# Performance work log

Hardware: AMD Instinct MI355X
Metric: run time of the kernel (lower is better)

Reference implementation:

```python
import jax, jax.numpy as jnp
import numpy as np

N_NODES = 30000
N_EDGES = 480000
IN_SIZE = 256
EDGE_FEAT = 32
N_TOWERS = 4
DELTA = 2.5


def setup_inputs():
    key = jax.random.key(0)
    ks = jax.random.split(key, 8)
    T, d = N_TOWERS, IN_SIZE // N_TOWERS
    m_in = 2 * d + EDGE_FEAT                 # M: Linear(2*tower_in+edge_feat -> tower_in)
    u_in = (4 * 3 + 1) * d                   # U: Linear((n_agg*n_scaler+1)*tower_in -> tower_out)
    return {
        "n_feat": jax.random.normal(ks[0], (N_NODES, IN_SIZE), jnp.float32),
        "e_feat": jax.random.normal(ks[1], (N_EDGES, EDGE_FEAT), jnp.float32),
        "src": jax.random.randint(ks[2], (N_EDGES,), 0, N_NODES),
        "dst": jax.random.randint(ks[3], (N_EDGES,), 0, N_NODES),
        "M_w": jax.random.normal(ks[4], (T, d, m_in), jnp.float32) * (1.0 / np.sqrt(m_in)),
        "M_b": jnp.zeros((T, d), jnp.float32),
        "U_w": jax.random.normal(ks[5], (T, d, u_in), jnp.float32) * (1.0 / np.sqrt(u_in)),
        "U_b": jnp.zeros((T, d), jnp.float32),
        "bn_gamma": jnp.ones((T, d), jnp.float32),
        "bn_beta": jnp.zeros((T, d), jnp.float32),
        "mix_w": jax.random.normal(ks[6], (IN_SIZE, IN_SIZE), jnp.float32) * (1.0 / np.sqrt(IN_SIZE)),
        "mix_b": jnp.zeros((IN_SIZE,), jnp.float32),
    }


def reference(n_feat, e_feat, src, dst, M_w, M_b, U_w, U_b, bn_gamma, bn_beta, mix_w, mix_b):
    N, F = n_feat.shape
    T, d, _ = M_w.shape
    E = src.shape[0]
    h = n_feat.reshape(N, T, d)                                   # towers split the feature dim
    ef = jnp.broadcast_to(e_feat[:, None, :], (E, T, e_feat.shape[1]))
    f = jnp.concatenate([h[src], h[dst], ef], axis=-1)            # [E,T,2d+ef]
    msg = jnp.einsum('eti,toi->eto', f, M_w) + M_b                # per-edge message, [E,T,d]

    deg = jax.ops.segment_sum(jnp.ones((E,), msg.dtype), dst, num_segments=N)  # in-degree
    degc = jnp.maximum(deg, 1.0)[:, None, None]
    s = jax.ops.segment_sum(msg, dst, num_segments=N)
    ssq = jax.ops.segment_sum(msg * msg, dst, num_segments=N)
    mean = s / degc
    var = jax.nn.relu(ssq / degc - mean * mean)                   # DGL aggregate_var
    std = jnp.sqrt(var + 1e-30)                                   # DGL aggregate_std
    has = (deg > 0.0)[:, None, None]
    mx = jnp.where(has, jax.ops.segment_max(msg, dst, num_segments=N), 0.0)
    mn = jnp.where(has, jax.ops.segment_min(msg, dst, num_segments=N), 0.0)
    agg = jnp.concatenate([mean, mx, mn, std], axis=-1)           # [N,T,4d]

    logd = jnp.log(deg + 1.0)
    amp = (logd / DELTA)[:, None, None]                            # amplification scaler
    att = jnp.where(deg > 0.0, DELTA / jnp.maximum(logd, 1e-12), 0.0)[:, None, None]  # attenuation
    hsc = jnp.concatenate([agg, agg * amp, agg * att], axis=-1)   # [N,T,12d]

    u_in = jnp.concatenate([h, hsc], axis=-1)                     # [N,T,13d]
    u = jnp.einsum('nti,toi->nto', u_in, U_w) + U_b               # [N,T,d]
    mu = jnp.mean(u, axis=0)
    v = jnp.mean((u - mu) ** 2, axis=0)
    u = (u - mu) / jnp.sqrt(v + 1e-5) * bn_gamma + bn_beta        # BatchNorm1d (training mode)

    h_cat = u.reshape(N, F)
    mixed = h_cat @ mix_w.T + mix_b
    mixed = jnp.where(mixed > 0, mixed, 0.01 * mixed)             # LeakyReLU mixing layer
    out = mixed + n_feat                                          # residual (in_size==out_size)
    return jax.nn.relu(out)                                       # last == 0 -> ReLU
```

## Files before the change

### kernel.cpp

```cpp
#include <hip/hip_runtime.h>
#include <math.h>

constexpr float DELTA_ = 2.5f;
#define BN_BLOCKS 512

typedef __attribute__((ext_vector_type(8))) short bf16x8;
typedef __attribute__((ext_vector_type(4))) float f32x4;
typedef __attribute__((ext_vector_type(2))) _Float16 half2_t;

#if defined(__has_builtin)
#if __has_builtin(__builtin_amdgcn_fdot2)
#define DOT2(a,b,c) __builtin_amdgcn_fdot2((a),(b),(c),false)
#endif
#endif
#ifndef DOT2
#define DOT2(a,b,c) fmaf((float)(a).x,(float)(b).x, fmaf((float)(a).y,(float)(b).y,(c)))
#endif

__device__ inline ushort bf16h(float x){
  union { float f; unsigned u; } v; v.f = x;
  unsigned r = v.u + 0x7fffu + ((v.u >> 16) & 1u);
  return (ushort)(r >> 16);
}
__device__ inline float bf16f(ushort h){
  union { unsigned u; float f; } v; v.u = ((unsigned)h) << 16;
  return v.f;
}

__global__ __launch_bounds__(256) void k_tU(const float* __restrict__ Uw, ushort* __restrict__ Wpk2){
  int i = blockIdx.x*256 + threadIdx.x;
  if (i >= 4*192*320) return;
  int k   = i % 320;
  int col = (i/320) % 192;
  int t   = i/(320*192);
  int path = col >> 6, o = col & 63;
  float v = 0.f;
  int src = -1;
  if (k < 64){ if (path == 0) src = k; }
  else        src = k + path*256;
  if (src >= 0) v = Uw[((size_t)(t*64 + o))*832 + src];
  Wpk2[i] = bf16h(v);
}

__global__ __launch_bounds__(256) void k_tMm(const float* __restrict__ mixw, ushort* __restrict__ Wm2){
  int i = blockIdx.x*256 + threadIdx.x;
  if (i >= 256*256) return;
  Wm2[i] = bf16h(mixw[i]);
}

__global__ __launch_bounds__(256) void k_tE(const float* __restrict__ Mw, _Float16* __restrict__ Mwefh){
  int i = blockIdx.x*256 + threadIdx.x;
  if (i >= 256*32) return;
  int k = i & 31, c = i >> 5;
  Mwefh[i] = (_Float16)Mw[(size_t)c*160 + 128 + k];
}

__global__ __launch_bounds__(256) void k_xh(const float* __restrict__ nf, ushort* __restrict__ X2, int N){
  for (long i = blockIdx.x*256 + threadIdx.x; i < (long)N*256; i += (long)gridDim.x*256){
    int n = (int)(i >> 8), c = (int)(i & 255);
    int t = c >> 6, d = c & 63;
    int j = d >> 3, pos = d & 7;
    float v = nf[i];
    ushort hi = bf16h(v);
    size_t base = (((size_t)n*4 + t)*40 + j)*16;
    X2[base + pos]     = hi;
    X2[base + 8 + pos] = bf16h(v - bf16f(hi));
  }
}

__global__ __launch_bounds__(256) void k_hist(const int* __restrict__ dstv, int* __restrict__ cnt, int E){
  int e = blockIdx.x*256 + threadIdx.x;
  if (e < E) atomicAdd(&cnt[dstv[e]], 1);
}

__global__ __launch_bounds__(256) void k_scan1(const int* __restrict__ cnt, int* __restrict__ offs,
                                               int* __restrict__ bsum, int N){
  __shared__ int lds[256];
  int i = threadIdx.x;
  int g = blockIdx.x*256 + i;
  int v = (g < N) ? cnt[g] : 0;
  int acc = v;
  lds[i] = acc; __syncthreads();
  for (int s = 1; s < 256; s <<= 1){
    int t = (i >= s) ? lds[i - s] : 0;
    __syncthreads();
    acc += t; lds[i] = acc;
    __syncthreads();
  }
  if (g < N) offs[g] = acc - v;
  if (i == 255) bsum[blockIdx.x] = acc;
}

__global__ __launch_bounds__(256) void k_scan2(int* __restrict__ bsum, int NB){
  __shared__ int lds[256];
  int i = threadIdx.x;
  int v = (i < NB) ? bsum[i] : 0;
  int acc = v;
  lds[i] = acc; __syncthreads();
  for (int s = 1; s < 256; s <<= 1){
    int t = (i >= s) ? lds[i - s] : 0;
    __syncthreads();
    acc += t; lds[i] = acc;
    __syncthreads();
  }
  if (i < NB) bsum[i] = acc - v;
}

__global__ __launch_bounds__(256) void k_scan3(int* __restrict__ offs, const int* __restrict__ bsum, int N, int E){
  int g = blockIdx.x*256 + threadIdx.x;
  if (g < N) offs[g] += bsum[blockIdx.x];
  if (g == 0) offs[N] = E;
}

__global__ __launch_bounds__(256) void k_fill(const int* __restrict__ dstv, const int* __restrict__ offs,
                                              int* __restrict__ cur, int* __restrict__ elist, int E){
  int e = blockIdx.x*256 + threadIdx.x;
  if (e < E){
    int d = dstv[e];
    elist[offs[d] + atomicAdd(&cur[d], 1)] = e;
  }
}

__global__ __launch_bounds__(256) void k_perm(const int* __restrict__ elist, const int* __restrict__ srcv,
                                              const float* __restrict__ efeat,
                                              int* __restrict__ esrc, _Float16* __restrict__ efh, int E){
  int g = blockIdx.x*256 + threadIdx.x;
  int pos = g >> 3;
  int q   = g & 7;
  if (pos >= E) return;
  int e = elist[pos];
  if (q == 0) esrc[pos] = srcv[e];
  float4 v = *(const float4*)(efeat + (size_t)e*32 + q*4);
  union { ushort4 u; _Float16 h[4]; } cv;
  cv.h[0] = (_Float16)v.x; cv.h[1] = (_Float16)v.y;
  cv.h[2] = (_Float16)v.z; cv.h[3] = (_Float16)v.w;
  *(ushort4*)(efh + (size_t)pos*32 + q*4) = cv.u;
}

__global__ __launch_bounds__(256) void k_ab(const float* __restrict__ nf, const float* __restrict__ Mw,
                                            const float* __restrict__ Mb,
                                            _Float16* __restrict__ A_h, float* __restrict__ B, int N){
  int c = threadIdx.x;
  int t = __builtin_amdgcn_readfirstlane(threadIdx.x >> 6);
  float ws[64], wd[64];
  const float* row = Mw + (size_t)c*160;
#pragma unroll
  for (int k = 0; k < 64; k += 4){
    float4 a = *(const float4*)(row + k);
    float4 b = *(const float4*)(row + 64 + k);
    ws[k]=a.x; ws[k+1]=a.y; ws[k+2]=a.z; ws[k+3]=a.w;
    wd[k]=b.x; wd[k+1]=b.y; wd[k+2]=b.z; wd[k+3]=b.w;
  }
  float bias = Mb[c];
  for (int n = blockIdx.x; n < N; n += gridDim.x){
    const float* h = nf + (size_t)n*256 + t*64;
    float sa = 0.f, sb = 0.f;
#pragma unroll
    for (int k = 0; k < 64; k += 4){
      float4 h4 = *(const float4*)(h + k);
      sa = fmaf(ws[k], h4.x, sa);  sb = fmaf(wd[k], h4.x, sb);
      sa = fmaf(ws[k+1], h4.y, sa); sb = fmaf(wd[k+1], h4.y, sb);
      sa = fmaf(ws[k+2], h4.z, sa); sb = fmaf(wd[k+2], h4.z, sb);
      sa = fmaf(ws[k+3], h4.w, sa); sb = fmaf(wd[k+3], h4.w, sb);
    }
    A_h[(size_t)n*256 + c] = (_Float16)sa;
    B[(size_t)n*256 + c] = sb + bias;
  }
}

__global__ __launch_bounds__(256) void k_agg(const int* __restrict__ offs, const int* __restrict__ esrc,
                                             const _Float16* __restrict__ efh,
                                             const _Float16* __restrict__ A_h, const float* __restrict__ B,
                                             const _Float16* __restrict__ Mwefh,
                                             ushort* __restrict__ X2, float* __restrict__ sc, int N){
  int c = threadIdx.x;
  union Wu { int4 i[4]; half2_t h[16]; } wr;
  {
    const int4* wp = (const int4*)(Mwefh + (size_t)c*32);
    wr.i[0] = wp[0]; wr.i[1] = wp[1]; wr.i[2] = wp[2]; wr.i[3] = wp[3];
  }

  int n = blockIdx.x;
  if (n >= N) return;
  int o0 = __builtin_amdgcn_readfirstlane(offs[n]);
  int o1 = __builtin_amdgcn_readfirstlane(offs[n+1]);
  int cnt = o1 - o0;
  float b0 = B[(size_t)n*256 + c];
  float s = 0.f, ss = 0.f, mx = -__builtin_huge_valf(), mn = __builtin_huge_valf();

  union Eu { int4 i[4]; half2_t h[16]; };

  int i = 0;
  for (; i + 4 <= cnt; i += 4){
    int p = o0 + i;
    int s0 = __builtin_amdgcn_readfirstlane(esrc[p+0]);
    int s1 = __builtin_amdgcn_readfirstlane(esrc[p+1]);
    int s2 = __builtin_amdgcn_readfirstlane(esrc[p+2]);
    int s3 = __builtin_amdgcn_readfirstlane(esrc[p+3]);
    Eu e0, e1, e2, e3;
    {
      const int4* p0 = (const int4*)(efh + (size_t)(p+0)*32);
      const int4* p1 = (const int4*)(efh + (size_t)(p+1)*32);
      const int4* p2 = (const int4*)(efh + (size_t)(p+2)*32);
      const int4* p3 = (const int4*)(efh + (size_t)(p+3)*32);
#pragma unroll
      for (int q = 0; q < 4; ++q){ e0.i[q]=p0[q]; e1.i[q]=p1[q]; e2.i[q]=p2[q]; e3.i[q]=p3[q]; }
    }
    float a0 = (float)A_h[(size_t)s0*256 + c];
    float a1 = (float)A_h[(size_t)s1*256 + c];
    float a2 = (float)A_h[(size_t)s2*256 + c];
    float a3 = (float)A_h[(size_t)s3*256 + c];
    float m0 = b0 + a0;
    float m1 = b0 + a1;
    float m2 = b0 + a2;
    float m3 = b0 + a3;
#pragma unroll
    for (int q = 0; q < 16; ++q){
      m0 = DOT2(e0.h[q], wr.h[q], m0);
      m1 = DOT2(e1.h[q], wr.h[q], m1);
      m2 = DOT2(e2.h[q], wr.h[q], m2);
      m3 = DOT2(e3.h[q], wr.h[q], m3);
    }
    s += m0; s += m1; s += m2; s += m3;
    ss = fmaf(m0, m0, ss); ss = fmaf(m1, m1, ss);
    ss = fmaf(m2, m2, ss); ss = fmaf(m3, m3, ss);
    mx = fmaxf(mx, fmaxf(fmaxf(m0, m1), fmaxf(m2, m3)));
    mn = fminf(mn, fminf(fminf(m0, m1), fminf(m2, m3)));
  }
  for (; i < cnt; ++i){
    int p = o0 + i;
    int sidx = __builtin_amdgcn_readfirstlane(esrc[p]);
    Eu e0;
    {
      const int4* p0 = (const int4*)(efh + (size_t)p*32);
#pragma unroll
      for (int q = 0; q < 4; ++q) e0.i[q] = p0[q];
    }
    float m = b0 + (float)A_h[(size_t)sidx*256 + c];
#pragma unroll
    for (int q = 0; q < 16; ++q) m = DOT2(e0.h[q], wr.h[q], m);
    s += m;
    ss = fmaf(m, m, ss);
    mx = fmaxf(mx, m);
    mn = fminf(mn, m);
  }

  float deg  = (float)cnt;
  float degc = fmaxf(deg, 1.f);
  float inv  = 1.f / degc;
  float mean = s * inv;
  float var  = fmaxf(ss * inv - mean*mean, 0.f);
  float sd   = sqrtf(var + 1e-30f);
  if (cnt == 0){ mx = 0.f; mn = 0.f; }

  int t = c >> 6, d = c & 63;
#define PUTX(SLOT, VAL) { int kk = 64 + (SLOT)*64 + d; int jj = kk >> 3, pp = kk & 7;      \
    size_t base = (((size_t)n*4 + t)*40 + jj)*16;                                          \
    ushort hi = bf16h(VAL);                                                                \
    X2[base + pp] = hi; X2[base + 8 + pp] = bf16h((VAL) - bf16f(hi)); }
  PUTX(0, mean) PUTX(1, mx) PUTX(2, mn) PUTX(3, sd)
#undef PUTX
  if (c == 0){
    float logd = logf(deg + 1.f);
    sc[(size_t)n*2]     = logd * (1.f / DELTA_);
    sc[(size_t)n*2 + 1] = (cnt > 0) ? (DELTA_ / fmaxf(logd, 1e-12f)) : 0.f;
  }
}

__global__ __launch_bounds__(256) void k_u(const ushort* __restrict__ X2, const ushort* __restrict__ Wpk2,
                                           const float* __restrict__ sc, const float* __restrict__ Ub,
                                           float* __restrict__ uout, int Nn){
  __shared__ float su[64][68];
  int tid = threadIdx.x;
  int t   = blockIdx.y;
  int nbase = blockIdx.x*64;
  int lane = tid & 63, wv = tid >> 6;
  int li = lane & 15, kc = lane >> 4;
  int cbase = wv*48;

  f32x4 acc[4][3];
#pragma unroll
  for (int ri = 0; ri < 4; ++ri)
#pragma unroll
    for (int ci = 0; ci < 3; ++ci) acc[ri][ci] = (f32x4)0.f;

  const ushort* wb = Wpk2 + (size_t)t*192*320;

#pragma unroll 2
  for (int kt = 0; kt < 10; ++kt){
    bf16x8 ah[4], al[4], bh[3];
#pragma unroll
    for (int ri = 0; ri < 4; ++ri){
      int row = nbase + ri*16 + li;
      if (row >= Nn) row = Nn - 1;
      const ushort* ap = X2 + (((size_t)row*4 + t)*40 + kt*4 + kc)*16;
      ah[ri] = *(const bf16x8*)(ap);
      al[ri] = *(const bf16x8*)(ap + 8);
    }
#pragma unroll
    for (int ci = 0; ci < 3; ++ci){
      int col = cbase + ci*16 + li;
      bh[ci] = *(const bf16x8*)(wb + (size_t)col*320 + kt*32 + kc*8);
    }
#pragma unroll
    for (int ci = 0; ci < 3; ++ci)
#pragma unroll
      for (int ri = 0; ri < 4; ++ri){
        acc[ri][ci] = __builtin_amdgcn_mfma_f32_16x16x32_bf16(ah[ri], bh[ci], acc[ri][ci], 0, 0, 0);
        acc[ri][ci] = __builtin_amdgcn_mfma_f32_16x16x32_bf16(al[ri], bh[ci], acc[ri][ci], 0, 0, 0);
      }
  }

#define Y1_STORE(CI, OB) { _Pragma("unroll") for (int ri = 0; ri < 4; ++ri)               \
    { _Pragma("unroll") for (int r = 0; r < 4; ++r)                                        \
      su[ri*16 + kc*4 + r][(OB) + li] = acc[ri][CI][r]; } }
#define Y_ADD(CI, OB, SCOFF) { _Pragma("unroll") for (int ri = 0; ri < 4; ++ri)           \
    { _Pragma("unroll") for (int r = 0; r < 4; ++r){                                       \
      int node = ri*16 + kc*4 + r;                                                        \
      int gn = nbase + node; int gnc = (gn < Nn) ? gn : (Nn - 1);                          \
      float scl = sc[(size_t)gnc*2 + (SCOFF)];                                            \
      su[node][(OB) + li] += scl * acc[ri][CI][r]; } } }

  if (wv == 0){ Y1_STORE(0, 0)  Y1_STORE(1, 16) Y1_STORE(2, 32) }
  else if (wv == 1){ Y1_STORE(0, 48) }
  __syncthreads();
  if (wv == 1){ Y_ADD(1, 0, 0)  Y_ADD(2, 16, 0) }
  else if (wv == 2){ Y_ADD(0, 32, 0) Y_ADD(1, 48, 0) }
  __syncthreads();
  if (wv == 2){ Y_ADD(2, 0, 1) }
  else if (wv == 3){ Y_ADD(0, 16, 1) Y_ADD(1, 32, 1) Y_ADD(2, 48, 1) }
  __syncthreads();
#undef Y1_STORE
#undef Y_ADD

  for (int idx = tid; idx < 64*16; idx += 256){
    int n = idx >> 4, o4 = (idx & 15)*4;
    int gn = nbase + n;
    if (gn < Nn){
      float4 v = *(float4*)(&su[n][o4]);
      const float* ubp = Ub + t*64 + o4;
      v.x += ubp[0]; v.y += ubp[1]; v.z += ubp[2]; v.w += ubp[3];
      *(float4*)(&uout[(size_t)gn*256 + t*64 + o4]) = v;
    }
  }
}

__global__ __launch_bounds__(256) void k_bnstat(const float* __restrict__ u, float* __restrict__ part, int N){
  int c = threadIdx.x;
  int b = blockIdx.x;
  float s = 0.f, ss = 0.f;
  for (int n = b; n < N; n += gridDim.x){
    float v = u[(size_t)n*256 + c];
    s += v;
    ss = fmaf(v, v, ss);
  }
  part[(size_t)b*512 + c]       = s;
  part[(size_t)b*512 + 256 + c] = ss;
}

__global__ __launch_bounds__(256) void k_bnfin(const float* __restrict__ part, const float* __restrict__ gam,
                                               const float* __restrict__ bet, float* __restrict__ bnsc, int N){
  int c = threadIdx.x;
  float s = 0.f, ss = 0.f;
  for (int b = 0; b < BN_BLOCKS; ++b){
    s  += part[(size_t)b*512 + c];
    ss += part[(size_t)b*512 + 256 + c];
  }
  float invN = 1.f / (float)N;
  float mu  = s * invN;
  float ex2 = ss * invN;
  float var = fmaxf(ex2 - mu*mu, 0.f);
  float inv = 1.f / sqrtf(var + 1e-5f);
  float scale = gam[c] * inv;
  bnsc[c]       = scale;
  bnsc[256 + c] = bet[c] - mu*scale;
}

__global__ __launch_bounds__(256) void k_xm(const float* __restrict__ u, const float* __restrict__ bnsc,
                                            ushort* __restrict__ X2m, int N){
  for (long i = blockIdx.x*256 + threadIdx.x; i < (long)N*256; i += (long)gridDim.x*256){
    int n = (int)(i >> 8), c = (int)(i & 255);
    float v = fmaf(u[i], bnsc[c], bnsc[256 + c]);
    int j = c >> 3, pos = c & 7;
    size_t base = ((size_t)n*32 + j)*16;
    ushort hi = bf16h(v);
    X2m[base + pos]     = hi;
    X2m[base + 8 + pos] = bf16h(v - bf16f(hi));
  }
}

__global__ __launch_bounds__(256) void k_mix(const ushort* __restrict__ X2m, const ushort* __restrict__ Wm2,
                                             const float* __restrict__ mixb, const float* __restrict__ nf,
                                             float* __restrict__ outp, int Nn){
  int tid = threadIdx.x;
  int nbase = blockIdx.x*64;
  int lane = tid & 63, wv = tid >> 6;
  int li = lane & 15, kc = lane >> 4;

  f32x4 acc[4][4];
#pragma unroll
  for (int ri = 0; ri < 4; ++ri)
#pragma unroll
    for (int ci = 0; ci < 4; ++ci) acc[ri][ci] = (f32x4)0.f;

#pragma unroll 2
  for (int kt = 0; kt < 8; ++kt){
    bf16x8 ah[4], al[4], bh[4];
#pragma unroll
    for (int ri = 0; ri < 4; ++ri){
      int row = nbase + ri*16 + li;
      if (row >= Nn) row = Nn - 1;
      const ushort* ap = X2m + (((size_t)row*32 + kt*4 + kc))*16;
      ah[ri] = *(const bf16x8*)(ap);
      al[ri] = *(const bf16x8*)(ap + 8);
    }
#pragma unroll
    for (int ci = 0; ci < 4; ++ci){
      int col = wv*64 + ci*16 + li;
      bh[ci] = *(const bf16x8*)(Wm2 + (size_t)col*256 + kt*32 + kc*8);
    }
#pragma unroll
    for (int ci = 0; ci < 4; ++ci)
#pragma unroll
      for (int ri = 0; ri < 4; ++ri){
        acc[ri][ci] = __builtin_amdgcn_mfma_f32_16x16x32_bf16(ah[ri], bh[ci], acc[ri][ci], 0, 0, 0);
        acc[ri][ci] = __builtin_amdgcn_mfma_f32_16x16x32_bf16(al[ri], bh[ci], acc[ri][ci], 0, 0, 0);
      }
  }

#pragma unroll
  for (int ri = 0; ri < 4; ++ri){
#pragma unroll
    for (int r = 0; r < 4; ++r){
      int node = ri*16 + kc*4 + r;
      int gn = nbase + node;
      if (gn < Nn){
#pragma unroll
        for (int ci = 0; ci < 4; ++ci){
          int col = wv*64 + ci*16 + li;
          float m = acc[ri][ci][r] + mixb[col];
          m = (m > 0.f) ? m : 0.01f*m;
          float o = m + nf[(size_t)gn*256 + col];
          outp[(size_t)gn*256 + col] = fmaxf(o, 0.f);
        }
      }
    }
  }
}

extern "C" void kernel_launch(void* const* d_in, const int* in_sizes, int n_in,
                              void* d_out, int out_size, void* d_ws, size_t ws_size,
                              hipStream_t stream){
  const float* nf   = (const float*)d_in[0];
  const float* ef   = (const float*)d_in[1];
  const int*   srcv = (const int*)  d_in[2];
  const int*   dstv = (const int*)  d_in[3];
  const float* Mw   = (const float*)d_in[4];
  const float* Mb   = (const float*)d_in[5];
  const float* Uw   = (const float*)d_in[6];
  const float* Ub   = (const float*)d_in[7];
  const float* gam  = (const float*)d_in[8];
  const float* bet  = (const float*)d_in[9];
  const float* mixw = (const float*)d_in[10];
  const float* mixb = (const float*)d_in[11];
  int N = in_sizes[0] / 256;
  int E = in_sizes[2];
  float* out = (float*)d_out;

  char* wp = (char*)d_ws;
  auto alloc = [&](size_t bytes){
    char* p = wp;
    wp += (bytes + 1023) & ~(size_t)1023;
    return (void*)p;
  };
  int*      cnt   = (int*)     alloc((size_t)N*4);
  int*      offs  = (int*)     alloc((size_t)(N+1)*4);
  int*      cur   = (int*)     alloc((size_t)N*4);
  int*      bsum  = (int*)     alloc(256*4);
  int*      elist = (int*)     alloc((size_t)E*4);
  int*      esrc  = (int*)     alloc((size_t)E*4);
  size_t ealias   = (size_t)E*32*2;
  size_t malias   = (size_t)N*512*2;
  char*     shbuf = (char*)    alloc(ealias > malias ? ealias : malias);
  _Float16* efh   = (_Float16*)shbuf;
  ushort*   X2m   = (ushort*)  shbuf;
  _Float16* A_h   = (_Float16*)alloc((size_t)N*256*2);
  float*    B     = (float*)   alloc((size_t)N*256*4);
  float*    sc    = (float*)   alloc((size_t)N*2*4);
  float*    part  = (float*)   alloc((size_t)BN_BLOCKS*512*4);
  float*    bnsc  = (float*)   alloc(512*4);
  ushort*   X2    = (ushort*)  alloc((size_t)N*4*40*16*2);
  ushort*   Wpk2  = (ushort*)  alloc((size_t)4*192*320*2);
  ushort*   Wm2   = (ushort*)  alloc((size_t)256*256*2);
  _Float16* Mwefh = (_Float16*)alloc((size_t)256*32*2);

  hipMemsetAsync(cnt,  0, (size_t)N*4,  stream);
  hipMemsetAsync(cur,  0, (size_t)N*4,  stream);

  k_tU  <<<(4*192*320 + 255)/256, 256, 0, stream>>>(Uw, Wpk2);
  k_tMm <<<(256*256 + 255)/256, 256, 0, stream>>>(mixw, Wm2);
  k_tE  <<<(256*32 + 255)/256, 256, 0, stream>>>(Mw, Mwefh);
  k_hist<<<(E + 255)/256, 256, 0, stream>>>(dstv, cnt, E);
  k_ab  <<<2048, 256, 0, stream>>>(nf, Mw, Mb, A_h, B, N);
  k_xh  <<<2048, 256, 0, stream>>>(nf, X2, N);

  int NB = (N + 255)/256;
  k_scan1<<<NB, 256, 0, stream>>>(cnt, offs, bsum, N);
  k_scan2<<<1, 256, 0, stream>>>(bsum, NB);
  k_scan3<<<NB, 256, 0, stream>>>(offs, bsum, N, E);
  k_fill <<<(E + 255)/256, 256, 0, stream>>>(dstv, offs, cur, elist, E);
  k_perm <<<(E*8 + 255)/256, 256, 0, stream>>>(elist, srcv, ef, esrc, efh, E);

  k_agg<<<N, 256, 0, stream>>>(offs, esrc, efh, A_h, B, Mwefh, X2, sc, N);

  dim3 ugrid((N + 63)/64, 4);
  k_u<<<ugrid, 256, 0, stream>>>(X2, Wpk2, sc, Ub, out, N);

  k_bnstat<<<BN_BLOCKS, 256, 0, stream>>>(out, part, N);
  k_bnfin <<<1, 256, 0, stream>>>(part, gam, bet, bnsc, N);
  k_xm   <<<2048, 256, 0, stream>>>(out, bnsc, X2m, N);
  k_mix  <<<(N + 63)/64, 256, 0, stream>>>(X2m, Wm2, mixb, nf, out, N);
}
```

Before: 493.8 us.

## Use MFMA for edge-feature messages, fold split into k_ab, fuse BN stats into k_u

```diff
diff --git a/kernel.cpp b/kernel.cpp
--- a/kernel.cpp
+++ b/kernel.cpp
@@ -2,20 +2,10 @@
 #include <math.h>
 
 constexpr float DELTA_ = 2.5f;
-#define BN_BLOCKS 512
 
 typedef __attribute__((ext_vector_type(8))) short bf16x8;
+typedef __attribute__((ext_vector_type(8))) _Float16 f16x8;
 typedef __attribute__((ext_vector_type(4))) float f32x4;
-typedef __attribute__((ext_vector_type(2))) _Float16 half2_t;
-
-#if defined(__has_builtin)
-#if __has_builtin(__builtin_amdgcn_fdot2)
-#define DOT2(a,b,c) __builtin_amdgcn_fdot2((a),(b),(c),false)
-#endif
-#endif
-#ifndef DOT2
-#define DOT2(a,b,c) fmaf((float)(a).x,(float)(b).x, fmaf((float)(a).y,(float)(b).y,(c)))
-#endif
 
 __device__ inline ushort bf16h(float x){
   union { float f; unsigned u; } v; v.f = x;
@@ -48,24 +38,15 @@
   Wm2[i] = bf16h(mixw[i]);
 }
 
-__global__ __launch_bounds__(256) void k_tE(const float* __restrict__ Mw, _Float16* __restrict__ Mwefh){
+__global__ __launch_bounds__(256) void k_tE2(const float* __restrict__ Mw, _Float16* __restrict__ Wefp){
   int i = blockIdx.x*256 + threadIdx.x;
-  if (i >= 256*32) return;
-  int k = i & 31, c = i >> 5;
-  Mwefh[i] = (_Float16)Mw[(size_t)c*160 + 128 + k];
-}
-
-__global__ __launch_bounds__(256) void k_xh(const float* __restrict__ nf, ushort* __restrict__ X2, int N){
-  for (long i = blockIdx.x*256 + threadIdx.x; i < (long)N*256; i += (long)gridDim.x*256){
-    int n = (int)(i >> 8), c = (int)(i & 255);
-    int t = c >> 6, d = c & 63;
-    int j = d >> 3, pos = d & 7;
-    float v = nf[i];
-    ushort hi = bf16h(v);
-    size_t base = (((size_t)n*4 + t)*40 + j)*16;
-    X2[base + pos]     = hi;
-    X2[base + 8 + pos] = bf16h(v - bf16f(hi));
-  }
+  if (i >= 16*64*8) return;
+  int j    = i & 7;
+  int lane = (i >> 3) & 63;
+  int cb   = i >> 9;
+  int ch = cb*16 + (lane & 15);
+  int k  = ((lane >> 4) & 3)*8 + j;
+  Wefp[i] = (_Float16)Mw[(size_t)ch*160 + 128 + k];
 }
 
 __global__ __launch_bounds__(256) void k_hist(const int* __restrict__ dstv, int* __restrict__ cnt, int E){
@@ -139,7 +120,8 @@
 
 __global__ __launch_bounds__(256) void k_ab(const float* __restrict__ nf, const float* __restrict__ Mw,
                                             const float* __restrict__ Mb,
-                                            _Float16* __restrict__ A_h, float* __restrict__ B, int N){
+                                            _Float16* __restrict__ A_h, float* __restrict__ B,
+                                            ushort* __restrict__ X2, int N){
   int c = threadIdx.x;
   int t = __builtin_amdgcn_readfirstlane(threadIdx.x >> 6);
   float ws[64], wd[64];
@@ -165,102 +147,112 @@
     }
     A_h[(size_t)n*256 + c] = (_Float16)sa;
     B[(size_t)n*256 + c] = sb + bias;
+    float v = nf[(size_t)n*256 + c];
+    ushort hi = bf16h(v);
+    int d = c & 63, j = d >> 3, pp = d & 7;
+    size_t base = (((size_t)n*4 + t)*40 + j)*16;
+    X2[base + pp]     = hi;
+    X2[base + 8 + pp] = bf16h(v - bf16f(hi));
   }
 }
 
 __global__ __launch_bounds__(256) void k_agg(const int* __restrict__ offs, const int* __restrict__ esrc,
                                              const _Float16* __restrict__ efh,
                                              const _Float16* __restrict__ A_h, const float* __restrict__ B,
-                                             const _Float16* __restrict__ Mwefh,
-                                             ushort* __restrict__ X2, float* __restrict__ sc, int N){
-  int c = threadIdx.x;
-  union Wu { int4 i[4]; half2_t h[16]; } wr;
-  {
-    const int4* wp = (const int4*)(Mwefh + (size_t)c*32);
-    wr.i[0] = wp[0]; wr.i[1] = wp[1]; wr.i[2] = wp[2]; wr.i[3] = wp[3];
-  }
-
+                                             const _Float16* __restrict__ Wefp,
+                                             ushort* __restrict__ X2, float* __restrict__ sc, int N, int E){
   int n = blockIdx.x;
   if (n >= N) return;
-  int o0 = __builtin_amdgcn_readfirstlane(offs[n]);
-  int o1 = __builtin_amdgcn_readfirstlane(offs[n+1]);
+  int tid = threadIdx.x;
+  int lane = tid & 63, wv = tid >> 6;
+  int li = lane & 15, kq = lane >> 4;
+
+  int o0 = offs[n], o1 = offs[n+1];
   int cnt = o1 - o0;
-  float b0 = B[(size_t)n*256 + c];
-  float s = 0.f, ss = 0.f, mx = -__builtin_huge_valf(), mn = __builtin_huge_valf();
-
-  union Eu { int4 i[4]; half2_t h[16]; };
-
-  int i = 0;
-  for (; i + 4 <= cnt; i += 4){
-    int p = o0 + i;
-    int s0 = __builtin_amdgcn_readfirstlane(esrc[p+0]);
-    int s1 = __builtin_amdgcn_readfirstlane(esrc[p+1]);
-    int s2 = __builtin_amdgcn_readfirstlane(esrc[p+2]);
-    int s3 = __builtin_amdgcn_readfirstlane(esrc[p+3]);
-    Eu e0, e1, e2, e3;
-    {
-      const int4* p0 = (const int4*)(efh + (size_t)(p+0)*32);
-      const int4* p1 = (const int4*)(efh + (size_t)(p+1)*32);
-      const int4* p2 = (const int4*)(efh + (size_t)(p+2)*32);
-      const int4* p3 = (const int4*)(efh + (size_t)(p+3)*32);
-#pragma unroll
-      for (int q = 0; q < 4; ++q){ e0.i[q]=p0[q]; e1.i[q]=p1[q]; e2.i[q]=p2[q]; e3.i[q]=p3[q]; }
-    }
-    float a0 = (float)A_h[(size_t)s0*256 + c];
-    float a1 = (float)A_h[(size_t)s1*256 + c];
-    float a2 = (float)A_h[(size_t)s2*256 + c];
-    float a3 = (float)A_h[(size_t)s3*256 + c];
-    float m0 = b0 + a0;
-    float m1 = b0 + a1;
-    float m2 = b0 + a2;
-    float m3 = b0 + a3;
-#pragma unroll
-    for (int q = 0; q < 16; ++q){
-      m0 = DOT2(e0.h[q], wr.h[q], m0);
-      m1 = DOT2(e1.h[q], wr.h[q], m1);
-      m2 = DOT2(e2.h[q], wr.h[q], m2);
-      m3 = DOT2(e3.h[q], wr.h[q], m3);
-    }
-    s += m0; s += m1; s += m2; s += m3;
-    ss = fmaf(m0, m0, ss); ss = fmaf(m1, m1, ss);
-    ss = fmaf(m2, m2, ss); ss = fmaf(m3, m3, ss);
-    mx = fmaxf(mx, fmaxf(fmaxf(m0, m1), fmaxf(m2, m3)));
-    mn = fminf(mn, fminf(fminf(m0, m1), fminf(m2, m3)));
-  }
-  for (; i < cnt; ++i){
-    int p = o0 + i;
-    int sidx = __builtin_amdgcn_readfirstlane(esrc[p]);
-    Eu e0;
-    {
-      const int4* p0 = (const int4*)(efh + (size_t)p*32);
-#pragma unroll
-      for (int q = 0; q < 4; ++q) e0.i[q] = p0[q];
-    }
-    float m = b0 + (float)A_h[(size_t)sidx*256 + c];
-#pragma unroll
-    for (int q = 0; q < 16; ++q) m = DOT2(e0.h[q], wr.h[q], m);
-    s += m;
-    ss = fmaf(m, m, ss);
-    mx = fmaxf(mx, m);
-    mn = fminf(mn, m);
-  }
-
-  float deg  = (float)cnt;
-  float degc = fmaxf(deg, 1.f);
-  float inv  = 1.f / degc;
-  float mean = s * inv;
-  float var  = fmaxf(ss * inv - mean*mean, 0.f);
-  float sd   = sqrtf(var + 1e-30f);
-  if (cnt == 0){ mx = 0.f; mn = 0.f; }
-
-  int t = c >> 6, d = c & 63;
-#define PUTX(SLOT, VAL) { int kk = 64 + (SLOT)*64 + d; int jj = kk >> 3, pp = kk & 7;      \
-    size_t base = (((size_t)n*4 + t)*40 + jj)*16;                                          \
-    ushort hi = bf16h(VAL);                                                                \
-    X2[base + pp] = hi; X2[base + 8 + pp] = bf16h((VAL) - bf16f(hi)); }
-  PUTX(0, mean) PUTX(1, mx) PUTX(2, mn) PUTX(3, sd)
+
+  f16x8 bf[4];
+#pragma unroll
+  for (int cbl = 0; cbl < 4; ++cbl)
+    bf[cbl] = *(const f16x8*)(Wefp + ((size_t)(wv*4 + cbl)*64 + lane)*8);
+
+  float b0[4];
+#pragma unroll
+  for (int cbl = 0; cbl < 4; ++cbl)
+    b0[cbl] = B[(size_t)n*256 + wv*64 + cbl*16 + li];
+
+  float s[4]  = {0.f,0.f,0.f,0.f};
+  float ss[4] = {0.f,0.f,0.f,0.f};
+  float mx[4], mn[4];
+#pragma unroll
+  for (int cbl = 0; cbl < 4; ++cbl){
+    mx[cbl] = -__builtin_huge_valf();
+    mn[cbl] =  __builtin_huge_valf();
+  }
+
+  for (int p = o0; p < o1; p += 16){
+    int posa = p + li; if (posa > E - 1) posa = E - 1;
+    f16x8 af = *(const f16x8*)(efh + (size_t)posa*32 + kq*8);
+    f32x4 ep0 = __builtin_amdgcn_mfma_f32_16x16x32_f16(af, bf[0], (f32x4)0.f, 0, 0, 0);
+    f32x4 ep1 = __builtin_amdgcn_mfma_f32_16x16x32_f16(af, bf[1], (f32x4)0.f, 0, 0, 0);
+    f32x4 ep2 = __builtin_amdgcn_mfma_f32_16x16x32_f16(af, bf[2], (f32x4)0.f, 0, 0, 0);
+    f32x4 ep3 = __builtin_amdgcn_mfma_f32_16x16x32_f16(af, bf[3], (f32x4)0.f, 0, 0, 0);
+#pragma unroll
+    for (int r = 0; r < 4; ++r){
+      int pr = p + kq*4 + r;
+      if (pr < o1){
+        int srcn = esrc[pr];
+        const _Float16* ap = A_h + (size_t)srcn*256 + wv*64 + li;
+        float a0 = (float)ap[0];
+        float a1 = (float)ap[16];
+        float a2 = (float)ap[32];
+        float a3 = (float)ap[48];
+        float m0 = ep0[r] + a0;
+        float m1 = ep1[r] + a1;
+        float m2 = ep2[r] + a2;
+        float m3 = ep3[r] + a3;
+        s[0] += m0; ss[0] = fmaf(m0, m0, ss[0]); mx[0] = fmaxf(mx[0], m0); mn[0] = fminf(mn[0], m0);
+        s[1] += m1; ss[1] = fmaf(m1, m1, ss[1]); mx[1] = fmaxf(mx[1], m1); mn[1] = fminf(mn[1], m1);
+        s[2] += m2; ss[2] = fmaf(m2, m2, ss[2]); mx[2] = fmaxf(mx[2], m2); mn[2] = fminf(mn[2], m2);
+        s[3] += m3; ss[3] = fmaf(m3, m3, ss[3]); mx[3] = fmaxf(mx[3], m3); mn[3] = fminf(mn[3], m3);
+      }
+    }
+  }
+
+#pragma unroll
+  for (int cbl = 0; cbl < 4; ++cbl){
+    s[cbl]  += __shfl_xor(s[cbl], 16);  s[cbl]  += __shfl_xor(s[cbl], 32);
+    ss[cbl] += __shfl_xor(ss[cbl], 16); ss[cbl] += __shfl_xor(ss[cbl], 32);
+    mx[cbl] = fmaxf(mx[cbl], __shfl_xor(mx[cbl], 16));
+    mx[cbl] = fmaxf(mx[cbl], __shfl_xor(mx[cbl], 32));
+    mn[cbl] = fminf(mn[cbl], __shfl_xor(mn[cbl], 16));
+    mn[cbl] = fminf(mn[cbl], __shfl_xor(mn[cbl], 32));
+  }
+
+  if (lane < 16){
+    float deg  = (float)cnt;
+    float degc = fmaxf(deg, 1.f);
+    float inv  = 1.f / degc;
+#pragma unroll
+    for (int cbl = 0; cbl < 4; ++cbl){
+      float b = b0[cbl];
+      float S  = fmaf(deg, b, s[cbl]);
+      float SS = fmaf(deg, b*b, fmaf(2.f*b, s[cbl], ss[cbl]));
+      float mean = S * inv;
+      float var  = fmaxf(SS * inv - mean*mean, 0.f);
+      float sd   = sqrtf(var + 1e-30f);
+      float MX = (cnt > 0) ? (b + mx[cbl]) : 0.f;
+      float MN = (cnt > 0) ? (b + mn[cbl]) : 0.f;
+      int d = cbl*16 + li;
+#define PUTX(SLOT, VAL) { int kk = 64 + (SLOT)*64 + d; int jj = kk >> 3, pp = kk & 7;     \
+      size_t base = (((size_t)n*4 + wv)*40 + jj)*16;                                       \
+      ushort hi2 = bf16h(VAL);                                                             \
+      X2[base + pp] = hi2; X2[base + 8 + pp] = bf16h((VAL) - bf16f(hi2)); }
+      PUTX(0, mean) PUTX(1, MX) PUTX(2, MN) PUTX(3, sd)
 #undef PUTX
-  if (c == 0){
+    }
+  }
+  if (tid == 0){
+    float deg = (float)cnt;
     float logd = logf(deg + 1.f);
     sc[(size_t)n*2]     = logd * (1.f / DELTA_);
     sc[(size_t)n*2 + 1] = (cnt > 0) ? (DELTA_ / fmaxf(logd, 1e-12f)) : 0.f;
@@ -269,8 +261,10 @@
 
 __global__ __launch_bounds__(256) void k_u(const ushort* __restrict__ X2, const ushort* __restrict__ Wpk2,
                                            const float* __restrict__ sc, const float* __restrict__ Ub,
-                                           float* __restrict__ uout, int Nn){
+                                           float* __restrict__ uout, float* __restrict__ part,
+                                           int Nn, int NBLK){
   __shared__ float su[64][68];
+  __shared__ float pbn[2][4][64];
   int tid = threadIdx.x;
   int t   = blockIdx.y;
   int nbase = blockIdx.x*64;
@@ -343,28 +337,41 @@
       *(float4*)(&uout[(size_t)gn*256 + t*64 + o4]) = v;
     }
   }
-}
-
-__global__ __launch_bounds__(256) void k_bnstat(const float* __restrict__ u, float* __restrict__ part, int N){
+
+  {
+    int cl = tid & 63, grp = tid >> 6;
+    float ubv = Ub[t*64 + cl];
+    float ps = 0.f, pss = 0.f;
+#pragma unroll
+    for (int q = 0; q < 16; ++q){
+      int nn = grp*16 + q;
+      if (nbase + nn < Nn){
+        float v = su[nn][cl] + ubv;
+        ps += v;
+        pss = fmaf(v, v, pss);
+      }
+    }
+    pbn[0][grp][cl] = ps;
+    pbn[1][grp][cl] = pss;
+  }
+  __syncthreads();
+  if (tid < 128){
+    int which = tid >> 6, cl = tid & 63;
+    float v = pbn[which][0][cl] + pbn[which][1][cl] + pbn[which][2][cl] + pbn[which][3][cl];
+    part[((size_t)t*NBLK + blockIdx.x)*128 + which*64 + cl] = v;
+  }
+}
+
+__global__ __launch_bounds__(256) void k_bnfin(const float* __restrict__ part, const float* __restrict__ gam,
+                                               const float* __restrict__ bet, float* __restrict__ bnsc,
+                                               int N, int NBLK){
   int c = threadIdx.x;
-  int b = blockIdx.x;
+  int t = c >> 6, cl = c & 63;
   float s = 0.f, ss = 0.f;
-  for (int n = b; n < N; n += gridDim.x){
-    float v = u[(size_t)n*256 + c];
-    s += v;
-    ss = fmaf(v, v, ss);
-  }
-  part[(size_t)b*512 + c]       = s;
-  part[(size_t)b*512 + 256 + c] = ss;
-}
-
-__global__ __launch_bounds__(256) void k_bnfin(const float* __restrict__ part, const float* __restrict__ gam,
-                                               const float* __restrict__ bet, float* __restrict__ bnsc, int N){
-  int c = threadIdx.x;
-  float s = 0.f, ss = 0.f;
-  for (int b = 0; b < BN_BLOCKS; ++b){
-    s  += part[(size_t)b*512 + c];
-    ss += part[(size_t)b*512 + 256 + c];
+  for (int b = 0; b < NBLK; ++b){
+    const float* pp = part + ((size_t)t*NBLK + b)*128;
+    s  += pp[cl];
+    ss += pp[64 + cl];
   }
   float invN = 1.f / (float)N;
   float mu  = s * invN;
@@ -466,6 +473,7 @@
   int N = in_sizes[0] / 256;
   int E = in_sizes[2];
   float* out = (float*)d_out;
+  int NBLK = (N + 63)/64;
 
   char* wp = (char*)d_ws;
   auto alloc = [&](size_t bytes){
@@ -487,22 +495,21 @@
   _Float16* A_h   = (_Float16*)alloc((size_t)N*256*2);
   float*    B     = (float*)   alloc((size_t)N*256*4);
   float*    sc    = (float*)   alloc((size_t)N*2*4);
-  float*    part  = (float*)   alloc((size_t)BN_BLOCKS*512*4);
+  float*    part  = (float*)   alloc((size_t)4*NBLK*128*4);
   float*    bnsc  = (float*)   alloc(512*4);
   ushort*   X2    = (ushort*)  alloc((size_t)N*4*40*16*2);
   ushort*   Wpk2  = (ushort*)  alloc((size_t)4*192*320*2);
   ushort*   Wm2   = (ushort*)  alloc((size_t)256*256*2);
-  _Float16* Mwefh = (_Float16*)alloc((size_t)256*32*2);
+  _Float16* Wefp  = (_Float16*)alloc((size_t)16*64*8*2);
 
   hipMemsetAsync(cnt,  0, (size_t)N*4,  stream);
   hipMemsetAsync(cur,  0, (size_t)N*4,  stream);
 
   k_tU  <<<(4*192*320 + 255)/256, 256, 0, stream>>>(Uw, Wpk2);
   k_tMm <<<(256*256 + 255)/256, 256, 0, stream>>>(mixw, Wm2);
-  k_tE  <<<(256*32 + 255)/256, 256, 0, stream>>>(Mw, Mwefh);
+  k_tE2 <<<(16*64*8 + 255)/256, 256, 0, stream>>>(Mw, Wefp);
   k_hist<<<(E + 255)/256, 256, 0, stream>>>(dstv, cnt, E);
-  k_ab  <<<2048, 256, 0, stream>>>(nf, Mw, Mb, A_h, B, N);
-  k_xh  <<<2048, 256, 0, stream>>>(nf, X2, N);
+  k_ab  <<<2048, 256, 0, stream>>>(nf, Mw, Mb, A_h, B, X2, N);
 
   int NB = (N + 255)/256;
   k_scan1<<<NB, 256, 0, stream>>>(cnt, offs, bsum, N);
@@ -511,13 +518,12 @@
   k_fill <<<(E + 255)/256, 256, 0, stream>>>(dstv, offs, cur, elist, E);
   k_perm <<<(E*8 + 255)/256, 256, 0, stream>>>(elist, srcv, ef, esrc, efh, E);
 
-  k_agg<<<N, 256, 0, stream>>>(offs, esrc, efh, A_h, B, Mwefh, X2, sc, N);
-
-  dim3 ugrid((N + 63)/64, 4);
-  k_u<<<ugrid, 256, 0, stream>>>(X2, Wpk2, sc, Ub, out, N);
-
-  k_bnstat<<<BN_BLOCKS, 256, 0, stream>>>(out, part, N);
-  k_bnfin <<<1, 256, 0, stream>>>(part, gam, bet, bnsc, N);
+  k_agg<<<N, 256, 0, stream>>>(offs, esrc, efh, A_h, B, Wefp, X2, sc, N, E);
+
+  dim3 ugrid(NBLK, 4);
+  k_u<<<ugrid, 256, 0, stream>>>(X2, Wpk2, sc, Ub, out, part, N, NBLK);
+
+  k_bnfin<<<1, 256, 0, stream>>>(part, gam, bet, bnsc, N, NBLK);
   k_xm   <<<2048, 256, 0, stream>>>(out, bnsc, X2m, N);
-  k_mix  <<<(N + 63)/64, 256, 0, stream>>>(X2m, Wm2, mixb, nf, out, N);
-}
+  k_mix  <<<NBLK, 256, 0, stream>>>(X2m, Wm2, mixb, nf, out, N);
+}
```

After: 632.0 us. 28.0% more time.
